# Kernel tuning notes

Measured on AMD Instinct MI355X. Metric: run time of the kernel, lower is better.

Reference implementation:

```python
import jax, jax.numpy as jnp
import numpy as np

NUM_NODES = 50000
NUM_EDGES = 800000
NUM_GRAPHS = 256
FEAT = 128
STATE = 64
ROUNDS = 4
M = 32


def setup_inputs() -> dict:
    key = jax.random.key(0)
    ks = jax.random.split(key, 12)
    x = jax.random.normal(ks[0], (NUM_NODES, FEAT), dtype=jnp.float32)
    edge_index = jax.random.randint(ks[1], (2, NUM_EDGES), 0, NUM_NODES, dtype=jnp.int64)
    batch = jnp.sort(jax.random.randint(ks[2], (NUM_NODES,), 0, NUM_GRAPHS, dtype=jnp.int64))
    s = 0.1  # weight init scale
    return {
        "x": x,
        "edge_index": edge_index,
        "batch": batch,
        "in_W": jax.random.normal(ks[3], (FEAT, STATE), dtype=jnp.float32) * s,
        "in_b": jnp.zeros((STATE,), dtype=jnp.float32),
        "msg_W": jax.random.normal(ks[4], (ROUNDS, STATE, STATE), dtype=jnp.float32) * s,
        "msg_b": jnp.zeros((ROUNDS, STATE), dtype=jnp.float32),
        "upd_W": jax.random.normal(ks[5], (ROUNDS, STATE, STATE), dtype=jnp.float32) * s,
        "upd_b": jnp.zeros((ROUNDS, STATE), dtype=jnp.float32),
        "mean_W": jax.random.normal(ks[6], (STATE, M), dtype=jnp.float32) * s,
        "mean_b": jnp.zeros((M,), dtype=jnp.float32),
        "logvar_W": jax.random.normal(ks[7], (STATE, M), dtype=jnp.float32) * s,
        "logvar_b": jnp.zeros((M,), dtype=jnp.float32),
    }


def reference(x, edge_index, batch, in_W, in_b, msg_W, msg_b, upd_W, upd_b,
              mean_W, mean_b, logvar_W, logvar_b):
    num_nodes = x.shape[0]
    src, dst = edge_index[0], edge_index[1]  # (to, from) -> gather src, scatter dst
    # input net (dropout is identity in eval mode)
    state = jax.nn.relu(x @ in_W + in_b)  # [N, S]
    for r in range(ROUNDS):
        message = jax.nn.relu(state @ msg_W[r] + msg_b[r])          # [N, S]
        gathered = message[src]                                       # [E, S] irregular gather
        aggregated = jax.ops.segment_sum(gathered, dst, num_segments=num_nodes)  # [N, S] scatter-add
        state = state + jax.nn.relu(aggregated @ upd_W[r] + upd_b[r])
    graph_state = jax.ops.segment_sum(state, batch, num_segments=NUM_GRAPHS)  # [G, S]
    mean = graph_state @ mean_W + mean_b                              # [G, M]
    log_var = jnp.clip(graph_state @ logvar_W + logvar_b, -20.0, 2.0)
    std = jnp.exp(0.5 * log_var)
    return jnp.stack([mean, std])  # [2, G, M] -> Normal(mean, std) params
```

## Files before the change

kernel.cpp:

```cpp
#include <hip/hip_runtime.h>
#include <math.h>

#define NODES  50000
#define EDGES  800000
#define GRAPHS 256
#define FEAT   128
#define STATE  64
#define M_OUT  32
#define ROUNDS 4
#define NT32   ((NODES + 31) / 32)
#define HALF   32
#define PLANE  (50000L * 32L)
#define CAP    64
#define OVFMAX 8192
#define NFILL  391
#define NFT    (NFILL * 256)

typedef unsigned short bfraw;

__device__ __forceinline__ float bf2f(bfraw u) {
    union { unsigned int i; float f; } v; v.i = ((unsigned int)u) << 16; return v.f;
}
__device__ __forceinline__ bfraw f2bf(float f) {
    union { float f; unsigned int i; } v; v.f = f;
    unsigned int r = v.i + 0x7FFF + ((v.i >> 16) & 1);
    return (bfraw)(r >> 16);
}
__device__ __forceinline__ int packbf(float lo, float hi) {
    return ((int)f2bf(hi) << 16) | (int)f2bf(lo);
}
__device__ __forceinline__ void addv8(float* acc, int4 v, float m) {
    union { int i; float f; } t;
    t.i = v.x << 16;                  acc[0] += t.f * m;
    t.i = v.x & (int)0xffff0000;      acc[1] += t.f * m;
    t.i = v.y << 16;                  acc[2] += t.f * m;
    t.i = v.y & (int)0xffff0000;      acc[3] += t.f * m;
    t.i = v.z << 16;                  acc[4] += t.f * m;
    t.i = v.z & (int)0xffff0000;      acc[5] += t.f * m;
    t.i = v.w << 16;                  acc[6] += t.f * m;
    t.i = v.w & (int)0xffff0000;      acc[7] += t.f * m;
}
__device__ __forceinline__ int4 pack8(const float* a) {
    int4 o;
    o.x = packbf(a[0], a[1]); o.y = packbf(a[2], a[3]);
    o.z = packbf(a[4], a[5]); o.w = packbf(a[6], a[7]);
    return o;
}

__device__ __forceinline__ void gather_to_lds(
    const int* __restrict__ cnt, const unsigned short* __restrict__ csr,
    const int* __restrict__ ovfc, const int* __restrict__ ovf,
    const bfraw* __restrict__ plane0, const bfraw* __restrict__ plane1,
    float* __restrict__ sa)
{
    float dummy = 0.f;
    {
        const bfraw* p = (threadIdx.x < 128) ? plane0 : plane1;
        long s = (long)blockIdx.x * 1024 + (long)(threadIdx.x & 127) * 8;
        if (s + 8 <= PLANE) {
            int4 a = *(const int4*)(p + s);
            union { int i; float f; } t; t.i = a.x << 16;
            dummy = t.f;
        }
    }

    const int row = threadIdx.x >> 3;
    const int q   = (threadIdx.x & 7) * 8;
    const int n   = blockIdx.x * 32 + row;
    const bfraw* plane = (q < HALF) ? plane0 : plane1;
    const int qq = (q < HALF) ? q : q - HALF;

    int cn = (n < NODES) ? cnt[n] : 0;
    if (cn > CAP) cn = CAP;
    int beg = n * CAP, end = beg + cn;

    float acc[8] = {0.f, 0.f, 0.f, 0.f, 0.f, 0.f, 0.f, 0.f};
    for (int i = beg; i < end; i += 8) {
        int last = end - 1;
        int i1 = i + 1 < last ? i + 1 : last;
        int i2 = i + 2 < last ? i + 2 : last;
        int i3 = i + 3 < last ? i + 3 : last;
        int i4 = i + 4 < last ? i + 4 : last;
        int i5 = i + 5 < last ? i + 5 : last;
        int i6 = i + 6 < last ? i + 6 : last;
        int i7 = i + 7 < last ? i + 7 : last;
        int s0 = csr[i],  s1 = csr[i1], s2 = csr[i2], s3 = csr[i3];
        int s4 = csr[i4], s5 = csr[i5], s6 = csr[i6], s7 = csr[i7];
        int4 v0 = *(const int4*)(plane + (long)s0 * HALF + qq);
        int4 v1 = *(const int4*)(plane + (long)s1 * HALF + qq);
        int4 v2 = *(const int4*)(plane + (long)s2 * HALF + qq);
        int4 v3 = *(const int4*)(plane + (long)s3 * HALF + qq);
        int4 v4 = *(const int4*)(plane + (long)s4 * HALF + qq);
        int4 v5 = *(const int4*)(plane + (long)s5 * HALF + qq);
        int4 v6 = *(const int4*)(plane + (long)s6 * HALF + qq);
        int4 v7 = *(const int4*)(plane + (long)s7 * HALF + qq);
        float m1 = (i + 1 < end) ? 1.f : 0.f;
        float m2 = (i + 2 < end) ? 1.f : 0.f;
        float m3 = (i + 3 < end) ? 1.f : 0.f;
        float m4 = (i + 4 < end) ? 1.f : 0.f;
        float m5 = (i + 5 < end) ? 1.f : 0.f;
        float m6 = (i + 6 < end) ? 1.f : 0.f;
        float m7 = (i + 7 < end) ? 1.f : 0.f;
        addv8(acc, v0, 1.f); addv8(acc, v1, m1);
        addv8(acc, v2, m2);  addv8(acc, v3, m3);
        addv8(acc, v4, m4);  addv8(acc, v5, m5);
        addv8(acc, v6, m6);  addv8(acc, v7, m7);
    }
    acc[0] += dummy * 0.0f;

    int oc = *ovfc;
    if (oc > 0) {
        if (oc > OVFMAX) oc = OVFMAX;
        for (int t = 0; t < oc; t++) {
            int pk = ovf[t];
            if ((pk >> 16) == n) {
                int4 v = *(const int4*)(plane + (long)(pk & 0xffff) * HALF + qq);
                addv8(acc, v, 1.f);
            }
        }
    }

    *(float4*)(sa + row * 68 + q)     = make_float4(acc[0], acc[1], acc[2], acc[3]);
    *(float4*)(sa + row * 68 + q + 4) = make_float4(acc[4], acc[5], acc[6], acc[7]);
}

__global__ __launch_bounds__(256) void k_in_msg(
    const int* __restrict__ ei, int* __restrict__ cnt,
    unsigned short* __restrict__ csr, int* __restrict__ ovfc, int* __restrict__ ovf,
    const float* __restrict__ x, const float* __restrict__ inW, const float* __restrict__ inb,
    const float* __restrict__ msgW, const float* __restrict__ msgb,
    float* __restrict__ state, bfraw* __restrict__ msg0, bfraw* __restrict__ msg1)
{
    __shared__ float sW[64 * STATE];
    __shared__ float sInb[STATE], sMsgb[STATE];
    __shared__ float sx[32 * 132];
    __shared__ float ss[32 * 68];

    if (blockIdx.x < NFILL) {
        const int t = blockIdx.x * 256 + threadIdx.x;
        int src[8], dst[8];
        #pragma unroll
        for (int k = 0; k < 8; k++) {
            int e = t + k * NFT;
            bool v = (e < EDGES);
            src[k] = v ? __builtin_nontemporal_load(ei + e) : 0;
            dst[k] = v ? __builtin_nontemporal_load(ei + EDGES + e) : -1;
        }
        int slot[8];
        #pragma unroll
        for (int k = 0; k < 8; k++)
            slot[k] = (dst[k] >= 0) ? atomicAdd(&cnt[dst[k]], 1) : 0;
        #pragma unroll
        for (int k = 0; k < 8; k++) {
            if (dst[k] < 0) continue;
            if (slot[k] < CAP) csr[(long)dst[k] * CAP + slot[k]] = (unsigned short)src[k];
            else { int o = atomicAdd(ovfc, 1); if (o < OVFMAX) ovf[o] = (dst[k] << 16) | src[k]; }
        }
        return;
    }

    const int bx  = blockIdx.x - NFILL;
    const int row = threadIdx.x >> 3;
    const int q8  = (threadIdx.x & 7) << 3;
    const int base = bx * 32;
    const int n = base + row;

    if (threadIdx.x < STATE) {
        sInb[threadIdx.x]  = inb[threadIdx.x];
        sMsgb[threadIdx.x] = msgb[threadIdx.x];
    }
    for (int i = threadIdx.x; i < 1024; i += 256) {
        int r = i >> 5, q = (i & 31) << 2;
        float4 v = make_float4(0.f, 0.f, 0.f, 0.f);
        if (base + r < NODES) v = *(const float4*)(x + (long)(base + r) * FEAT + q);
        *(float4*)(sx + r * 132 + q) = v;
    }
    for (int i = threadIdx.x; i < 1024; i += 256)
        *(float4*)(sW + i * 4) = *(const float4*)(inW + i * 4);
    __syncthreads();

    float a[8];
    #pragma unroll
    for (int j = 0; j < 8; j++) a[j] = sInb[q8 + j];
    const float* xr = sx + row * 132;
    #pragma unroll 8
    for (int k = 0; k < 64; k++) {
        float xv = xr[k];
        float4 w0 = *(const float4*)(sW + k * STATE + q8);
        float4 w1 = *(const float4*)(sW + k * STATE + q8 + 4);
        a[0] += xv * w0.x; a[1] += xv * w0.y; a[2] += xv * w0.z; a[3] += xv * w0.w;
        a[4] += xv * w1.x; a[5] += xv * w1.y; a[6] += xv * w1.z; a[7] += xv * w1.w;
    }
    __syncthreads();
    for (int i = threadIdx.x; i < 1024; i += 256)
        *(float4*)(sW + i * 4) = *(const float4*)(inW + 64 * STATE + i * 4);
    __syncthreads();
    #pragma unroll 8
    for (int k = 0; k < 64; k++) {
        float xv = xr[64 + k];
        float4 w0 = *(const float4*)(sW + k * STATE + q8);
        float4 w1 = *(const float4*)(sW + k * STATE + q8 + 4);
        a[0] += xv * w0.x; a[1] += xv * w0.y; a[2] += xv * w0.z; a[3] += xv * w0.w;
        a[4] += xv * w1.x; a[5] += xv * w1.y; a[6] += xv * w1.z; a[7] += xv * w1.w;
    }
    #pragma unroll
    for (int j = 0; j < 8; j++) a[j] = fmaxf(a[j], 0.f);
    if (n < NODES) {
        *(float4*)(state + (long)n * STATE + q8)     = make_float4(a[0], a[1], a[2], a[3]);
        *(float4*)(state + (long)n * STATE + q8 + 4) = make_float4(a[4], a[5], a[6], a[7]);
    }
    *(float4*)(ss + row * 68 + q8)     = make_float4(a[0], a[1], a[2], a[3]);
    *(float4*)(ss + row * 68 + q8 + 4) = make_float4(a[4], a[5], a[6], a[7]);
    __syncthreads();
    for (int i = threadIdx.x; i < 1024; i += 256)
        *(float4*)(sW + i * 4) = *(const float4*)(msgW + i * 4);
    __syncthreads();

    float m[8];
    #pragma unroll
    for (int j = 0; j < 8; j++) m[j] = sMsgb[q8 + j];
    const float* sr = ss + row * 68;
    #pragma unroll 8
    for (int k = 0; k < STATE; k++) {
        float sv = sr[k];
        float4 w0 = *(const float4*)(sW + k * STATE + q8);
        float4 w1 = *(const float4*)(sW + k * STATE + q8 + 4);
        m[0] += sv * w0.x; m[1] += sv * w0.y; m[2] += sv * w0.z; m[3] += sv * w0.w;
        m[4] += sv * w1.x; m[5] += sv * w1.y; m[6] += sv * w1.z; m[7] += sv * w1.w;
    }
    #pragma unroll
    for (int j = 0; j < 8; j++) m[j] = fmaxf(m[j], 0.f);
    if (n < NODES) {
        bfraw* dst = (q8 < HALF) ? (msg0 + (long)n * HALF + q8) : (msg1 + (long)n * HALF + (q8 - HALF));
        *(int4*)dst = pack8(m);
    }
}

__global__ __launch_bounds__(256) void k_round_msg(
    const int* __restrict__ cnt, const unsigned short* __restrict__ csr,
    const int* __restrict__ ovfc, const int* __restrict__ ovf,
    const bfraw* __restrict__ plane0, const bfraw* __restrict__ plane1,
    const float* __restrict__ updW, const float* __restrict__ updb,
    const float* __restrict__ msgW, const float* __restrict__ msgb,
    float* __restrict__ state, bfraw* __restrict__ msg0, bfraw* __restrict__ msg1)
{
    __shared__ float sW[64 * STATE];
    __shared__ float sUpdb[STATE], sMsgb[STATE];
    __shared__ float sa[32 * 68];

    const int row = threadIdx.x >> 3;
    const int q8  = (threadIdx.x & 7) << 3;
    const int n = blockIdx.x * 32 + row;

    if (threadIdx.x < STATE) {
        sUpdb[threadIdx.x] = updb[threadIdx.x];
        sMsgb[threadIdx.x] = msgb[threadIdx.x];
    }
    for (int i = threadIdx.x; i < 1024; i += 256)
        *(float4*)(sW + i * 4) = *(const float4*)(updW + i * 4);

    gather_to_lds(cnt, csr, ovfc, ovf, plane0, plane1, sa);
    __syncthreads();

    float a[8];
    #pragma unroll
    for (int j = 0; j < 8; j++) a[j] = sUpdb[q8 + j];
    const float* ar = sa + row * 68;
    #pragma unroll 8
    for (int k = 0; k < STATE; k++) {
        float av = ar[k];
        float4 w0 = *(const float4*)(sW + k * STATE + q8);
        float4 w1 = *(const float4*)(sW + k * STATE + q8 + 4);
        a[0] += av * w0.x; a[1] += av * w0.y; a[2] += av * w0.z; a[3] += av * w0.w;
        a[4] += av * w1.x; a[5] += av * w1.y; a[6] += av * w1.z; a[7] += av * w1.w;
    }
    #pragma unroll
    for (int j = 0; j < 8; j++) a[j] = fmaxf(a[j], 0.f);
    float s[8] = {0.f,0.f,0.f,0.f,0.f,0.f,0.f,0.f};
    if (n < NODES) {
        float4 st0 = *(const float4*)(state + (long)n * STATE + q8);
        float4 st1 = *(const float4*)(state + (long)n * STATE + q8 + 4);
        s[0] = st0.x + a[0]; s[1] = st0.y + a[1]; s[2] = st0.z + a[2]; s[3] = st0.w + a[3];
        s[4] = st1.x + a[4]; s[5] = st1.y + a[5]; s[6] = st1.z + a[6]; s[7] = st1.w + a[7];
        *(float4*)(state + (long)n * STATE + q8)     = make_float4(s[0], s[1], s[2], s[3]);
        *(float4*)(state + (long)n * STATE + q8 + 4) = make_float4(s[4], s[5], s[6], s[7]);
    }
    __syncthreads();
    *(float4*)(sa + row * 68 + q8)     = make_float4(s[0], s[1], s[2], s[3]);
    *(float4*)(sa + row * 68 + q8 + 4) = make_float4(s[4], s[5], s[6], s[7]);
    for (int i = threadIdx.x; i < 1024; i += 256)
        *(float4*)(sW + i * 4) = *(const float4*)(msgW + i * 4);
    __syncthreads();

    float m[8];
    #pragma unroll
    for (int j = 0; j < 8; j++) m[j] = sMsgb[q8 + j];
    const float* sr = sa + row * 68;
    #pragma unroll 8
    for (int k = 0; k < STATE; k++) {
        float sv = sr[k];
        float4 w0 = *(const float4*)(sW + k * STATE + q8);
        float4 w1 = *(const float4*)(sW + k * STATE + q8 + 4);
        m[0] += sv * w0.x; m[1] += sv * w0.y; m[2] += sv * w0.z; m[3] += sv * w0.w;
        m[4] += sv * w1.x; m[5] += sv * w1.y; m[6] += sv * w1.z; m[7] += sv * w1.w;
    }
    #pragma unroll
    for (int j = 0; j < 8; j++) m[j] = fmaxf(m[j], 0.f);
    if (n < NODES) {
        bfraw* dst = (q8 < HALF) ? (msg0 + (long)n * HALF + q8) : (msg1 + (long)n * HALF + (q8 - HALF));
        *(int4*)dst = pack8(m);
    }
}

__global__ __launch_bounds__(256) void k_round_pool(
    const int* __restrict__ cnt, const unsigned short* __restrict__ csr,
    const int* __restrict__ ovfc, const int* __restrict__ ovf,
    const bfraw* __restrict__ plane0, const bfraw* __restrict__ plane1,
    const float* __restrict__ updW, const float* __restrict__ updb,
    const float* __restrict__ state, const int* __restrict__ batch,
    float* __restrict__ gs)
{
    __shared__ float sW[64 * STATE];
    __shared__ float sUpdb[STATE];
    __shared__ float sa[32 * 68];
    __shared__ int   sg[32];

    const int row = threadIdx.x >> 3;
    const int q8  = (threadIdx.x & 7) << 3;
    const int base = blockIdx.x * 32;
    const int n = base + row;

    if (threadIdx.x < STATE) sUpdb[threadIdx.x] = updb[threadIdx.x];
    for (int i = threadIdx.x; i < 1024; i += 256)
        *(float4*)(sW + i * 4) = *(const float4*)(updW + i * 4);
    if (threadIdx.x < 32) {
        int nn = base + threadIdx.x;
        sg[threadIdx.x] = batch[nn < NODES ? nn : NODES - 1];
    }

    gather_to_lds(cnt, csr, ovfc, ovf, plane0, plane1, sa);
    __syncthreads();

    float a[8];
    #pragma unroll
    for (int j = 0; j < 8; j++) a[j] = sUpdb[q8 + j];
    const float* ar = sa + row * 68;
    #pragma unroll 8
    for (int k = 0; k < STATE; k++) {
        float av = ar[k];
        float4 w0 = *(const float4*)(sW + k * STATE + q8);
        float4 w1 = *(const float4*)(sW + k * STATE + q8 + 4);
        a[0] += av * w0.x; a[1] += av * w0.y; a[2] += av * w0.z; a[3] += av * w0.w;
        a[4] += av * w1.x; a[5] += av * w1.y; a[6] += av * w1.z; a[7] += av * w1.w;
    }
    float s[8] = {0.f,0.f,0.f,0.f,0.f,0.f,0.f,0.f};
    if (n < NODES) {
        float4 st0 = *(const float4*)(state + (long)n * STATE + q8);
        float4 st1 = *(const float4*)(state + (long)n * STATE + q8 + 4);
        s[0] = st0.x + fmaxf(a[0], 0.f); s[1] = st0.y + fmaxf(a[1], 0.f);
        s[2] = st0.z + fmaxf(a[2], 0.f); s[3] = st0.w + fmaxf(a[3], 0.f);
        s[4] = st1.x + fmaxf(a[4], 0.f); s[5] = st1.y + fmaxf(a[5], 0.f);
        s[6] = st1.z + fmaxf(a[6], 0.f); s[7] = st1.w + fmaxf(a[7], 0.f);
    }
    __syncthreads();
    *(float4*)(sa + row * 68 + q8)     = make_float4(s[0], s[1], s[2], s[3]);
    *(float4*)(sa + row * 68 + q8 + 4) = make_float4(s[4], s[5], s[6], s[7]);
    __syncthreads();

    if (threadIdx.x < STATE) {
        const int f = threadIdx.x;
        float run = sa[f];
        int g = sg[0];
        #pragma unroll
        for (int r = 1; r < 32; r++) {
            int g2 = sg[r];
            float v = sa[r * 68 + f];
            if (g2 != g) {
                atomicAdd(&gs[g * STATE + f], run);
                run = v; g = g2;
            } else {
                run += v;
            }
        }
        atomicAdd(&gs[g * STATE + f], run);
    }
}

__global__ __launch_bounds__(64) void k_final(
    const float* __restrict__ gs,
    const float* __restrict__ meanW, const float* __restrict__ meanb,
    const float* __restrict__ lvW, const float* __restrict__ lvb,
    float* __restrict__ out)
{
    __shared__ float row[STATE];
    const int g = blockIdx.x;
    const int j = threadIdx.x;
    row[j] = gs[g * STATE + j];
    __syncthreads();
    if (j < M_OUT) {
        float acc = meanb[j];
        #pragma unroll
        for (int k = 0; k < STATE; k++) acc += row[k] * meanW[k * M_OUT + j];
        out[g * M_OUT + j] = acc;
    } else {
        int jj = j - M_OUT;
        float acc = lvb[jj];
        #pragma unroll
        for (int k = 0; k < STATE; k++) acc += row[k] * lvW[k * M_OUT + jj];
        acc = fminf(fmaxf(acc, -20.f), 2.f);
        out[GRAPHS * M_OUT + g * M_OUT + jj] = expf(0.5f * acc);
    }
}

extern "C" void kernel_launch(void* const* d_in, const int* in_sizes, int n_in,
                              void* d_out, int out_size, void* d_ws, size_t ws_size,
                              hipStream_t stream) {
    const float* x     = (const float*)d_in[0];
    const int*   ei    = (const int*)d_in[1];
    const int*   batch = (const int*)d_in[2];
    const float* inW   = (const float*)d_in[3];
    const float* inb   = (const float*)d_in[4];
    const float* msgW  = (const float*)d_in[5];
    const float* msgb  = (const float*)d_in[6];
    const float* updW  = (const float*)d_in[7];
    const float* updb  = (const float*)d_in[8];
    const float* meanW = (const float*)d_in[9];
    const float* meanb = (const float*)d_in[10];
    const float* lvW   = (const float*)d_in[11];
    const float* lvb   = (const float*)d_in[12];
    float* out = (float*)d_out;

    const size_t NS   = (size_t)NODES * STATE * sizeof(float);
    const size_t PLB  = (size_t)PLANE * sizeof(bfraw);
    char* ws = (char*)d_ws;
    size_t off = 0;
    auto alloc = [&](size_t bytes) { void* p = ws + off; off += (bytes + 255) & ~(size_t)255; return p; };
    float* state  = (float*)alloc(NS);
    bfraw* msgA0  = (bfraw*)alloc(PLB);
    bfraw* msgA1  = (bfraw*)alloc(PLB);
    bfraw* msgB0  = (bfraw*)alloc(PLB);
    bfraw* msgB1  = (bfraw*)alloc(PLB);
    float* gs     = (float*)alloc((size_t)GRAPHS * STATE * sizeof(float));
    int*   cnt    = (int*)alloc((size_t)NODES * sizeof(int));
    int*   ovfc   = (int*)alloc(256);
    int*   ovf    = (int*)alloc((size_t)OVFMAX * sizeof(int));
    unsigned short* csr = (unsigned short*)alloc((size_t)NODES * CAP * sizeof(unsigned short));

    hipMemsetAsync(cnt, 0, (size_t)NODES * sizeof(int), stream);
    hipMemsetAsync(ovfc, 0, sizeof(int), stream);
    hipMemsetAsync(gs, 0, (size_t)GRAPHS * STATE * sizeof(float), stream);

    k_in_msg<<<NFILL + NT32, 256, 0, stream>>>(ei, cnt, csr, ovfc, ovf,
                                               x, inW, inb, msgW, msgb, state, msgA0, msgA1);

    bfraw *mi0 = msgA0, *mi1 = msgA1, *mo0 = msgB0, *mo1 = msgB1;
    for (int r = 0; r < ROUNDS; r++) {
        if (r < ROUNDS - 1) {
            k_round_msg<<<NT32, 256, 0, stream>>>(
                cnt, csr, ovfc, ovf, mi0, mi1,
                updW + r * STATE * STATE, updb + r * STATE,
                msgW + (r + 1) * STATE * STATE, msgb + (r + 1) * STATE,
                state, mo0, mo1);
            bfraw* t0 = mi0; mi0 = mo0; mo0 = t0;
            bfraw* t1 = mi1; mi1 = mo1; mo1 = t1;
        } else {
            k_round_pool<<<NT32, 256, 0, stream>>>(
                cnt, csr, ovfc, ovf, mi0, mi1,
                updW + r * STATE * STATE, updb + r * STATE,
                state, batch, gs);
        }
    }

    k_final<<<GRAPHS, 64, 0, stream>>>(gs, meanW, meanb, lvW, lvb, out);
}
```

Baseline: 300.8 us.

## Use 64-node blocks, vectorized CSR index loads, and direct x reads

Round kernels now process 64 nodes per 512-thread block, so each weight matrix load into LDS is amortised over twice as many nodes. The neighbour gather reads CSR indices as two 16-byte vectors covering 16 neighbours and issues up to 16 independent row loads per iteration, which raises memory-level parallelism over the previous 8 scalar index loads. The input kernel drops its LDS staging of x and reads each row directly with float4 loads. The costs are larger LDS per block and fewer blocks, which may lower occupancy, plus more register pressure from holding 16 int4 values.

Measured after the change: 447.3 us. 48.7% more time.

```diff
diff --git a/kernel.cpp b/kernel.cpp
--- a/kernel.cpp
+++ b/kernel.cpp
@@ -9,6 +9,7 @@
 #define M_OUT  32
 #define ROUNDS 4
 #define NT32   ((NODES + 31) / 32)
+#define NT64   ((NODES + 63) / 64)
 #define HALF   32
 #define PLANE  (50000L * 32L)
 #define CAP    64
@@ -18,9 +19,6 @@
 
 typedef unsigned short bfraw;
 
-__device__ __forceinline__ float bf2f(bfraw u) {
-    union { unsigned int i; float f; } v; v.i = ((unsigned int)u) << 16; return v.f;
-}
 __device__ __forceinline__ bfraw f2bf(float f) {
     union { float f; unsigned int i; } v; v.f = f;
     unsigned int r = v.i + 0x7FFF + ((v.i >> 16) & 1);
@@ -47,7 +45,7 @@
     return o;
 }
 
-__device__ __forceinline__ void gather_to_lds(
+__device__ __forceinline__ void gather_to_lds64(
     const int* __restrict__ cnt, const unsigned short* __restrict__ csr,
     const int* __restrict__ ovfc, const int* __restrict__ ovf,
     const bfraw* __restrict__ plane0, const bfraw* __restrict__ plane1,
@@ -55,8 +53,8 @@
 {
     float dummy = 0.f;
     {
-        const bfraw* p = (threadIdx.x < 128) ? plane0 : plane1;
-        long s = (long)blockIdx.x * 1024 + (long)(threadIdx.x & 127) * 8;
+        const bfraw* p = (threadIdx.x & 256) ? plane1 : plane0;
+        long s = (long)blockIdx.x * 2048 + (long)(threadIdx.x & 255) * 8;
         if (s + 8 <= PLANE) {
             int4 a = *(const int4*)(p + s);
             union { int i; float f; } t; t.i = a.x << 16;
@@ -66,45 +64,48 @@
 
     const int row = threadIdx.x >> 3;
     const int q   = (threadIdx.x & 7) * 8;
-    const int n   = blockIdx.x * 32 + row;
+    const int n   = blockIdx.x * 64 + row;
     const bfraw* plane = (q < HALF) ? plane0 : plane1;
     const int qq = (q < HALF) ? q : q - HALF;
 
     int cn = (n < NODES) ? cnt[n] : 0;
     if (cn > CAP) cn = CAP;
-    int beg = n * CAP, end = beg + cn;
+    const unsigned short* crow = csr + (long)n * CAP;
 
     float acc[8] = {0.f, 0.f, 0.f, 0.f, 0.f, 0.f, 0.f, 0.f};
-    for (int i = beg; i < end; i += 8) {
-        int last = end - 1;
-        int i1 = i + 1 < last ? i + 1 : last;
-        int i2 = i + 2 < last ? i + 2 : last;
-        int i3 = i + 3 < last ? i + 3 : last;
-        int i4 = i + 4 < last ? i + 4 : last;
-        int i5 = i + 5 < last ? i + 5 : last;
-        int i6 = i + 6 < last ? i + 6 : last;
-        int i7 = i + 7 < last ? i + 7 : last;
-        int s0 = csr[i],  s1 = csr[i1], s2 = csr[i2], s3 = csr[i3];
-        int s4 = csr[i4], s5 = csr[i5], s6 = csr[i6], s7 = csr[i7];
-        int4 v0 = *(const int4*)(plane + (long)s0 * HALF + qq);
-        int4 v1 = *(const int4*)(plane + (long)s1 * HALF + qq);
-        int4 v2 = *(const int4*)(plane + (long)s2 * HALF + qq);
-        int4 v3 = *(const int4*)(plane + (long)s3 * HALF + qq);
-        int4 v4 = *(const int4*)(plane + (long)s4 * HALF + qq);
-        int4 v5 = *(const int4*)(plane + (long)s5 * HALF + qq);
-        int4 v6 = *(const int4*)(plane + (long)s6 * HALF + qq);
-        int4 v7 = *(const int4*)(plane + (long)s7 * HALF + qq);
-        float m1 = (i + 1 < end) ? 1.f : 0.f;
-        float m2 = (i + 2 < end) ? 1.f : 0.f;
-        float m3 = (i + 3 < end) ? 1.f : 0.f;
-        float m4 = (i + 4 < end) ? 1.f : 0.f;
-        float m5 = (i + 5 < end) ? 1.f : 0.f;
-        float m6 = (i + 6 < end) ? 1.f : 0.f;
-        float m7 = (i + 7 < end) ? 1.f : 0.f;
-        addv8(acc, v0, 1.f); addv8(acc, v1, m1);
-        addv8(acc, v2, m2);  addv8(acc, v3, m3);
-        addv8(acc, v4, m4);  addv8(acc, v5, m5);
-        addv8(acc, v6, m6);  addv8(acc, v7, m7);
+    for (int i = 0; i < cn; i += 16) {
+        int4 ia = *(const int4*)(crow + i);
+        int4 ib = *(const int4*)(crow + i + 8);
+        int rem = cn - i;
+        int idx[16];
+        idx[0]  = ia.x & 0xffff; idx[1]  = ((unsigned)ia.x) >> 16;
+        idx[2]  = ia.y & 0xffff; idx[3]  = ((unsigned)ia.y) >> 16;
+        idx[4]  = ia.z & 0xffff; idx[5]  = ((unsigned)ia.z) >> 16;
+        idx[6]  = ia.w & 0xffff; idx[7]  = ((unsigned)ia.w) >> 16;
+        idx[8]  = ib.x & 0xffff; idx[9]  = ((unsigned)ib.x) >> 16;
+        idx[10] = ib.y & 0xffff; idx[11] = ((unsigned)ib.y) >> 16;
+        idx[12] = ib.z & 0xffff; idx[13] = ((unsigned)ib.z) >> 16;
+        idx[14] = ib.w & 0xffff; idx[15] = ((unsigned)ib.w) >> 16;
+
+        int4 v[16];
+        #pragma unroll
+        for (int j = 0; j < 8; j++) {
+            int s_ = (j < rem) ? idx[j] : idx[0];
+            v[j] = *(const int4*)(plane + (long)s_ * HALF + qq);
+        }
+        if (rem > 8) {
+            #pragma unroll
+            for (int j = 8; j < 16; j++) {
+                int s_ = (j < rem) ? idx[j] : idx[0];
+                v[j] = *(const int4*)(plane + (long)s_ * HALF + qq);
+            }
+        }
+        #pragma unroll
+        for (int j = 0; j < 8; j++) addv8(acc, v[j], (j < rem) ? 1.f : 0.f);
+        if (rem > 8) {
+            #pragma unroll
+            for (int j = 8; j < 16; j++) addv8(acc, v[j], (j < rem) ? 1.f : 0.f);
+        }
     }
     acc[0] += dummy * 0.0f;
 
@@ -133,7 +134,6 @@
 {
     __shared__ float sW[64 * STATE];
     __shared__ float sInb[STATE], sMsgb[STATE];
-    __shared__ float sx[32 * 132];
     __shared__ float ss[32 * 68];
 
     if (blockIdx.x < NFILL) {
@@ -164,17 +164,12 @@
     const int q8  = (threadIdx.x & 7) << 3;
     const int base = bx * 32;
     const int n = base + row;
+    const float* xrow = x + (long)((n < NODES) ? n : 0) * FEAT;
 
     if (threadIdx.x < STATE) {
         sInb[threadIdx.x]  = inb[threadIdx.x];
         sMsgb[threadIdx.x] = msgb[threadIdx.x];
     }
-    for (int i = threadIdx.x; i < 1024; i += 256) {
-        int r = i >> 5, q = (i & 31) << 2;
-        float4 v = make_float4(0.f, 0.f, 0.f, 0.f);
-        if (base + r < NODES) v = *(const float4*)(x + (long)(base + r) * FEAT + q);
-        *(float4*)(sx + r * 132 + q) = v;
-    }
     for (int i = threadIdx.x; i < 1024; i += 256)
         *(float4*)(sW + i * 4) = *(const float4*)(inW + i * 4);
     __syncthreads();
@@ -182,26 +177,35 @@
     float a[8];
     #pragma unroll
     for (int j = 0; j < 8; j++) a[j] = sInb[q8 + j];
-    const float* xr = sx + row * 132;
-    #pragma unroll 8
-    for (int k = 0; k < 64; k++) {
-        float xv = xr[k];
-        float4 w0 = *(const float4*)(sW + k * STATE + q8);
-        float4 w1 = *(const float4*)(sW + k * STATE + q8 + 4);
-        a[0] += xv * w0.x; a[1] += xv * w0.y; a[2] += xv * w0.z; a[3] += xv * w0.w;
-        a[4] += xv * w1.x; a[5] += xv * w1.y; a[6] += xv * w1.z; a[7] += xv * w1.w;
+    #pragma unroll
+    for (int k4 = 0; k4 < 16; k4++) {
+        float4 xv = *(const float4*)(xrow + (k4 << 2));
+        const int kb = k4 << 2;
+        float xs[4] = {xv.x, xv.y, xv.z, xv.w};
+        #pragma unroll
+        for (int c = 0; c < 4; c++) {
+            float4 w0 = *(const float4*)(sW + (kb + c) * STATE + q8);
+            float4 w1 = *(const float4*)(sW + (kb + c) * STATE + q8 + 4);
+            a[0] += xs[c] * w0.x; a[1] += xs[c] * w0.y; a[2] += xs[c] * w0.z; a[3] += xs[c] * w0.w;
+            a[4] += xs[c] * w1.x; a[5] += xs[c] * w1.y; a[6] += xs[c] * w1.z; a[7] += xs[c] * w1.w;
+        }
     }
     __syncthreads();
     for (int i = threadIdx.x; i < 1024; i += 256)
         *(float4*)(sW + i * 4) = *(const float4*)(inW + 64 * STATE + i * 4);
     __syncthreads();
-    #pragma unroll 8
-    for (int k = 0; k < 64; k++) {
-        float xv = xr[64 + k];
-        float4 w0 = *(const float4*)(sW + k * STATE + q8);
-        float4 w1 = *(const float4*)(sW + k * STATE + q8 + 4);
-        a[0] += xv * w0.x; a[1] += xv * w0.y; a[2] += xv * w0.z; a[3] += xv * w0.w;
-        a[4] += xv * w1.x; a[5] += xv * w1.y; a[6] += xv * w1.z; a[7] += xv * w1.w;
+    #pragma unroll
+    for (int k4 = 0; k4 < 16; k4++) {
+        float4 xv = *(const float4*)(xrow + 64 + (k4 << 2));
+        const int kb = k4 << 2;
+        float xs[4] = {xv.x, xv.y, xv.z, xv.w};
+        #pragma unroll
+        for (int c = 0; c < 4; c++) {
+            float4 w0 = *(const float4*)(sW + (kb + c) * STATE + q8);
+            float4 w1 = *(const float4*)(sW + (kb + c) * STATE + q8 + 4);
+            a[0] += xs[c] * w0.x; a[1] += xs[c] * w0.y; a[2] += xs[c] * w0.z; a[3] += xs[c] * w0.w;
+            a[4] += xs[c] * w1.x; a[5] += xs[c] * w1.y; a[6] += xs[c] * w1.z; a[7] += xs[c] * w1.w;
+        }
     }
     #pragma unroll
     for (int j = 0; j < 8; j++) a[j] = fmaxf(a[j], 0.f);
@@ -236,7 +240,7 @@
     }
 }
 
-__global__ __launch_bounds__(256) void k_round_msg(
+__global__ __launch_bounds__(512) void k_round_msg(
     const int* __restrict__ cnt, const unsigned short* __restrict__ csr,
     const int* __restrict__ ovfc, const int* __restrict__ ovf,
     const bfraw* __restrict__ plane0, const bfraw* __restrict__ plane1,
@@ -246,20 +250,20 @@
 {
     __shared__ float sW[64 * STATE];
     __shared__ float sUpdb[STATE], sMsgb[STATE];
-    __shared__ float sa[32 * 68];
+    __shared__ float sa[64 * 68];
 
     const int row = threadIdx.x >> 3;
     const int q8  = (threadIdx.x & 7) << 3;
-    const int n = blockIdx.x * 32 + row;
+    const int n = blockIdx.x * 64 + row;
 
     if (threadIdx.x < STATE) {
         sUpdb[threadIdx.x] = updb[threadIdx.x];
         sMsgb[threadIdx.x] = msgb[threadIdx.x];
     }
-    for (int i = threadIdx.x; i < 1024; i += 256)
+    for (int i = threadIdx.x; i < 1024; i += 512)
         *(float4*)(sW + i * 4) = *(const float4*)(updW + i * 4);
 
-    gather_to_lds(cnt, csr, ovfc, ovf, plane0, plane1, sa);
+    gather_to_lds64(cnt, csr, ovfc, ovf, plane0, plane1, sa);
     __syncthreads();
 
     float a[8];
@@ -288,7 +292,7 @@
     __syncthreads();
     *(float4*)(sa + row * 68 + q8)     = make_float4(s[0], s[1], s[2], s[3]);
     *(float4*)(sa + row * 68 + q8 + 4) = make_float4(s[4], s[5], s[6], s[7]);
-    for (int i = threadIdx.x; i < 1024; i += 256)
+    for (int i = threadIdx.x; i < 1024; i += 512)
         *(float4*)(sW + i * 4) = *(const float4*)(msgW + i * 4);
     __syncthreads();
 
@@ -312,7 +316,7 @@
     }
 }
 
-__global__ __launch_bounds__(256) void k_round_pool(
+__global__ __launch_bounds__(512) void k_round_pool(
     const int* __restrict__ cnt, const unsigned short* __restrict__ csr,
     const int* __restrict__ ovfc, const int* __restrict__ ovf,
     const bfraw* __restrict__ plane0, const bfraw* __restrict__ plane1,
@@ -322,23 +326,23 @@
 {
     __shared__ float sW[64 * STATE];
     __shared__ float sUpdb[STATE];
-    __shared__ float sa[32 * 68];
-    __shared__ int   sg[32];
+    __shared__ float sa[64 * 68];
+    __shared__ int   sg[64];
 
     const int row = threadIdx.x >> 3;
     const int q8  = (threadIdx.x & 7) << 3;
-    const int base = blockIdx.x * 32;
+    const int base = blockIdx.x * 64;
     const int n = base + row;
 
     if (threadIdx.x < STATE) sUpdb[threadIdx.x] = updb[threadIdx.x];
-    for (int i = threadIdx.x; i < 1024; i += 256)
+    for (int i = threadIdx.x; i < 1024; i += 512)
         *(float4*)(sW + i * 4) = *(const float4*)(updW + i * 4);
-    if (threadIdx.x < 32) {
+    if (threadIdx.x < 64) {
         int nn = base + threadIdx.x;
         sg[threadIdx.x] = batch[nn < NODES ? nn : NODES - 1];
     }
 
-    gather_to_lds(cnt, csr, ovfc, ovf, plane0, plane1, sa);
+    gather_to_lds64(cnt, csr, ovfc, ovf, plane0, plane1, sa);
     __syncthreads();
 
     float a[8];
@@ -372,7 +376,7 @@
         float run = sa[f];
         int g = sg[0];
         #pragma unroll
-        for (int r = 1; r < 32; r++) {
+        for (int r = 1; r < 64; r++) {
             int g2 = sg[r];
             float v = sa[r * 68 + f];
             if (g2 != g) {
@@ -456,7 +460,7 @@
     bfraw *mi0 = msgA0, *mi1 = msgA1, *mo0 = msgB0, *mo1 = msgB1;
     for (int r = 0; r < ROUNDS; r++) {
         if (r < ROUNDS - 1) {
-            k_round_msg<<<NT32, 256, 0, stream>>>(
+            k_round_msg<<<NT64, 512, 0, stream>>>(
                 cnt, csr, ovfc, ovf, mi0, mi1,
                 updW + r * STATE * STATE, updb + r * STATE,
                 msgW + (r + 1) * STATE * STATE, msgb + (r + 1) * STATE,
@@ -464,7 +468,7 @@
             bfraw* t0 = mi0; mi0 = mo0; mo0 = t0;
             bfraw* t1 = mi1; mi1 = mo1; mo1 = t1;
         } else {
-            k_round_pool<<<NT32, 256, 0, stream>>>(
+            k_round_pool<<<NT64, 512, 0, stream>>>(
                 cnt, csr, ovfc, ovf, mi0, mi1,
                 updW + r * STATE * STATE, updb + r * STATE,
                 state, batch, gs);
```

## Vectorize CSR index loads in gather and shrink shared memory in input kernel

Applied to the files above, without the earlier changes.

The aggregation loop now loads eight 16-bit neighbor indices with one 128-bit load from the fixed-stride CSR row, replacing eight scalar loads and clamped index arithmetic. Masked-off lanes reuse the first index. The input/message kernel splits the x tile into two 64-column halves that share one buffer with the state tile, cutting shared memory per block to raise occupancy. The cost is an extra global load phase of x between the two matmul halves.

New measurement: 302.2 us. No clear change (+0.4%).

```diff
diff --git a/kernel.cpp b/kernel.cpp
--- a/kernel.cpp
+++ b/kernel.cpp
@@ -18,9 +18,6 @@
 
 typedef unsigned short bfraw;
 
-__device__ __forceinline__ float bf2f(bfraw u) {
-    union { unsigned int i; float f; } v; v.i = ((unsigned int)u) << 16; return v.f;
-}
 __device__ __forceinline__ bfraw f2bf(float f) {
     union { float f; unsigned int i; } v; v.f = f;
     unsigned int r = v.i + 0x7FFF + ((v.i >> 16) & 1);
@@ -72,39 +69,25 @@
 
     int cn = (n < NODES) ? cnt[n] : 0;
     if (cn > CAP) cn = CAP;
-    int beg = n * CAP, end = beg + cn;
+    const unsigned short* crow = csr + (long)n * CAP;
 
     float acc[8] = {0.f, 0.f, 0.f, 0.f, 0.f, 0.f, 0.f, 0.f};
-    for (int i = beg; i < end; i += 8) {
-        int last = end - 1;
-        int i1 = i + 1 < last ? i + 1 : last;
-        int i2 = i + 2 < last ? i + 2 : last;
-        int i3 = i + 3 < last ? i + 3 : last;
-        int i4 = i + 4 < last ? i + 4 : last;
-        int i5 = i + 5 < last ? i + 5 : last;
-        int i6 = i + 6 < last ? i + 6 : last;
-        int i7 = i + 7 < last ? i + 7 : last;
-        int s0 = csr[i],  s1 = csr[i1], s2 = csr[i2], s3 = csr[i3];
-        int s4 = csr[i4], s5 = csr[i5], s6 = csr[i6], s7 = csr[i7];
-        int4 v0 = *(const int4*)(plane + (long)s0 * HALF + qq);
-        int4 v1 = *(const int4*)(plane + (long)s1 * HALF + qq);
-        int4 v2 = *(const int4*)(plane + (long)s2 * HALF + qq);
-        int4 v3 = *(const int4*)(plane + (long)s3 * HALF + qq);
-        int4 v4 = *(const int4*)(plane + (long)s4 * HALF + qq);
-        int4 v5 = *(const int4*)(plane + (long)s5 * HALF + qq);
-        int4 v6 = *(const int4*)(plane + (long)s6 * HALF + qq);
-        int4 v7 = *(const int4*)(plane + (long)s7 * HALF + qq);
-        float m1 = (i + 1 < end) ? 1.f : 0.f;
-        float m2 = (i + 2 < end) ? 1.f : 0.f;
-        float m3 = (i + 3 < end) ? 1.f : 0.f;
-        float m4 = (i + 4 < end) ? 1.f : 0.f;
-        float m5 = (i + 5 < end) ? 1.f : 0.f;
-        float m6 = (i + 6 < end) ? 1.f : 0.f;
-        float m7 = (i + 7 < end) ? 1.f : 0.f;
-        addv8(acc, v0, 1.f); addv8(acc, v1, m1);
-        addv8(acc, v2, m2);  addv8(acc, v3, m3);
-        addv8(acc, v4, m4);  addv8(acc, v5, m5);
-        addv8(acc, v6, m6);  addv8(acc, v7, m7);
+    for (int i = 0; i < cn; i += 8) {
+        int4 ia = *(const int4*)(crow + i);
+        int rem = cn - i;
+        int idx[8];
+        idx[0] = ia.x & 0xffff; idx[1] = ((unsigned)ia.x) >> 16;
+        idx[2] = ia.y & 0xffff; idx[3] = ((unsigned)ia.y) >> 16;
+        idx[4] = ia.z & 0xffff; idx[5] = ((unsigned)ia.z) >> 16;
+        idx[6] = ia.w & 0xffff; idx[7] = ((unsigned)ia.w) >> 16;
+        int4 v[8];
+        #pragma unroll
+        for (int j = 0; j < 8; j++) {
+            int s_ = (j < rem) ? idx[j] : idx[0];
+            v[j] = *(const int4*)(plane + (long)s_ * HALF + qq);
+        }
+        #pragma unroll
+        for (int j = 0; j < 8; j++) addv8(acc, v[j], (j < rem) ? 1.f : 0.f);
     }
     acc[0] += dummy * 0.0f;
 
@@ -132,9 +115,8 @@
     float* __restrict__ state, bfraw* __restrict__ msg0, bfraw* __restrict__ msg1)
 {
     __shared__ float sW[64 * STATE];
+    __shared__ float sB[32 * 68];
     __shared__ float sInb[STATE], sMsgb[STATE];
-    __shared__ float sx[32 * 132];
-    __shared__ float ss[32 * 68];
 
     if (blockIdx.x < NFILL) {
         const int t = blockIdx.x * 256 + threadIdx.x;
@@ -169,11 +151,11 @@
         sInb[threadIdx.x]  = inb[threadIdx.x];
         sMsgb[threadIdx.x] = msgb[threadIdx.x];
     }
-    for (int i = threadIdx.x; i < 1024; i += 256) {
-        int r = i >> 5, q = (i & 31) << 2;
+    for (int i = threadIdx.x; i < 512; i += 256) {
+        int r = i >> 4, q = (i & 15) << 2;
         float4 v = make_float4(0.f, 0.f, 0.f, 0.f);
         if (base + r < NODES) v = *(const float4*)(x + (long)(base + r) * FEAT + q);
-        *(float4*)(sx + r * 132 + q) = v;
+        *(float4*)(sB + r * 68 + q) = v;
     }
     for (int i = threadIdx.x; i < 1024; i += 256)
         *(float4*)(sW + i * 4) = *(const float4*)(inW + i * 4);
@@ -182,7 +164,7 @@
     float a[8];
     #pragma unroll
     for (int j = 0; j < 8; j++) a[j] = sInb[q8 + j];
-    const float* xr = sx + row * 132;
+    const float* xr = sB + row * 68;
     #pragma unroll 8
     for (int k = 0; k < 64; k++) {
         float xv = xr[k];
@@ -192,12 +174,18 @@
         a[4] += xv * w1.x; a[5] += xv * w1.y; a[6] += xv * w1.z; a[7] += xv * w1.w;
     }
     __syncthreads();
+    for (int i = threadIdx.x; i < 512; i += 256) {
+        int r = i >> 4, q = (i & 15) << 2;
+        float4 v = make_float4(0.f, 0.f, 0.f, 0.f);
+        if (base + r < NODES) v = *(const float4*)(x + (long)(base + r) * FEAT + 64 + q);
+        *(float4*)(sB + r * 68 + q) = v;
+    }
     for (int i = threadIdx.x; i < 1024; i += 256)
         *(float4*)(sW + i * 4) = *(const float4*)(inW + 64 * STATE + i * 4);
     __syncthreads();
     #pragma unroll 8
     for (int k = 0; k < 64; k++) {
-        float xv = xr[64 + k];
+        float xv = xr[k];
         float4 w0 = *(const float4*)(sW + k * STATE + q8);
         float4 w1 = *(const float4*)(sW + k * STATE + q8 + 4);
         a[0] += xv * w0.x; a[1] += xv * w0.y; a[2] += xv * w0.z; a[3] += xv * w0.w;
@@ -209,9 +197,9 @@
         *(float4*)(state + (long)n * STATE + q8)     = make_float4(a[0], a[1], a[2], a[3]);
         *(float4*)(state + (long)n * STATE + q8 + 4) = make_float4(a[4], a[5], a[6], a[7]);
     }
-    *(float4*)(ss + row * 68 + q8)     = make_float4(a[0], a[1], a[2], a[3]);
-    *(float4*)(ss + row * 68 + q8 + 4) = make_float4(a[4], a[5], a[6], a[7]);
-    __syncthreads();
+    __syncthreads();
+    *(float4*)(sB + row * 68 + q8)     = make_float4(a[0], a[1], a[2], a[3]);
+    *(float4*)(sB + row * 68 + q8 + 4) = make_float4(a[4], a[5], a[6], a[7]);
     for (int i = threadIdx.x; i < 1024; i += 256)
         *(float4*)(sW + i * 4) = *(const float4*)(msgW + i * 4);
     __syncthreads();
@@ -219,7 +207,7 @@
     float m[8];
     #pragma unroll
     for (int j = 0; j < 8; j++) m[j] = sMsgb[q8 + j];
-    const float* sr = ss + row * 68;
+    const float* sr = sB + row * 68;
     #pragma unroll 8
     for (int k = 0; k < STATE; k++) {
         float sv = sr[k];
```
